# Kernel tuning notes

Hardware: AMD Instinct MI355X
Metric: run time of the kernel (lower is better)

Reference implementation:

```python
import jax, jax.numpy as jnp
from jax import lax
import numpy as np

B, T, U, P, K = 8192, 256, 64, 64, 2048

def setup_inputs() -> dict:
    key = jax.random.key(0)
    ku, ky, kw1, kw2 = jax.random.split(key, 4)
    u = jax.random.normal(ku, (B, T, U), dtype=jnp.float32)
    y0 = jax.random.normal(ky, (B, P), dtype=jnp.float32)
    W1 = jax.random.normal(kw1, (U + P, K), dtype=jnp.float32) * (1.0 / np.sqrt(U + P))
    b1 = jnp.zeros((K,), dtype=jnp.float32)
    W2 = jax.random.normal(kw2, (K, 1), dtype=jnp.float32) * (1.0 / np.sqrt(K))
    b2 = jnp.zeros((1,), dtype=jnp.float32)
    return {"u": u, "y0": y0, "W1": W1, "b1": b1, "W2": W2, "b2": b2}

def reference(u, y0, W1, b1, W2, b2):
    def step(y, u_t):
        # x: [B, U+P]
        x = jnp.concatenate([u_t, y], axis=1)
        h = jnp.tanh(x @ W1 + b1)          # [B, K]
        pred = h @ W2 + b2                 # [B, 1]
        # roll(shift=1)[:,1:] == y[:, :-1]; newest prediction goes to front
        y_new = jnp.concatenate([pred, y[:, :-1]], axis=1)  # [B, P]
        return y_new, pred

    u_t_first = jnp.swapaxes(u, 0, 1)      # [T, B, U]
    _, preds = lax.scan(step, y0, u_t_first)  # preds: [T, B, 1]
    return jnp.transpose(preds, (1, 0, 2))    # [B, T, 1]
```

## Files before the change

### kernel.cpp

```cpp
#include <hip/hip_runtime.h>
#include <hip/hip_fp16.h>
#include <cstdint>
#include <cstddef>

#define T_STEPS 256
#define K_DIM 2048
#define NCW 8
#define NT_W 8
#define REG_NT 4
#define LDS_NT 4

typedef _Float16 f16;
typedef _Float16 f16x8 __attribute__((ext_vector_type(8)));
typedef _Float16 f16x4 __attribute__((ext_vector_type(4)));
typedef _Float16 f16x2 __attribute__((ext_vector_type(2)));
typedef float f32x4 __attribute__((ext_vector_type(4)));

#define W1S_OFF 0
#define U_OFF   131072
#define Y_OFF   139264
#define PB_OFF  155648
#define SMEM_BYTES 157696

#define W1P_BYTES (128 * 4 * 64 * 16)
#define MBOX_OFF  W1P_BYTES
#define MBOX_BYTES (256 * 2 * 2 * 32 * 8)

__global__ void __launch_bounds__(64) prepack_w1(const float* __restrict__ W1,
                                                 f16* __restrict__ w1p) {
  int blk = blockIdx.x;
  int ntile = blk >> 2, ks = blk & 3;
  int lane = threadIdx.x;
  int col = ntile * 16 + (lane & 15);
  int kb = ks * 32 + ((lane >> 4) << 3);
  f16x8 pk;
#pragma unroll
  for (int i = 0; i < 8; ++i) pk[i] = (f16)W1[(size_t)(kb + i) * K_DIM + col];
  ((f16x8*)w1p)[(ntile * 4 + ks) * 64 + lane] = pk;
}

__global__ void __launch_bounds__(512, 2)
__attribute__((amdgpu_waves_per_eu(2, 2)))
rnn_fused(const float* __restrict__ u, const float* __restrict__ y0,
          const f16* __restrict__ w1p, const float* __restrict__ b1,
          const float* __restrict__ w2, const float* __restrict__ b2,
          float* __restrict__ out, unsigned long long* mbox)
{
  __shared__ __align__(16) char smem[SMEM_BYTES];
  f16x8* w1s     = (f16x8*)(smem + W1S_OFF);
  float* predbuf = (float*)(smem + PB_OFF);

  const int tid = threadIdx.x, lane = tid & 63, wave = tid >> 6;
  const int b = blockIdx.x;
  const int jj_ = b >> 3;
  const int half = jj_ & 1;
  const int pair = ((b & 7) << 4) | (jj_ >> 1);
  const int partner = b ^ 8;
  const int row0 = pair * 64;
  const int colbase = half * 1024;
  const float b2v = b2[0];
  const f16x8* w1pv = (const f16x8*)w1p;
  const float TWO_L = 2.885390081777927f;

  float b1x[NT_W], w2v[NT_W];
#pragma unroll
  for (int nt = 0; nt < NT_W; ++nt) {
    int col = colbase + wave * 128 + nt * 16 + (lane & 15);
    b1x[nt] = TWO_L * b1[col];
    w2v[nt] = w2[col];
  }

  float Chalf = 0.f;
  if (wave == 0) {
    float s = 0.f;
#pragma unroll
    for (int i = 0; i < 16; ++i) s += w2[colbase + lane * 16 + i];
    s += __shfl_xor(s, 1);  s += __shfl_xor(s, 2);  s += __shfl_xor(s, 4);
    s += __shfl_xor(s, 8);  s += __shfl_xor(s, 16); s += __shfl_xor(s, 32);
    Chalf = s;
  }

  f16x8 w1r[REG_NT * 4];
#pragma unroll
  for (int nt = 0; nt < REG_NT; ++nt)
#pragma unroll
    for (int ks = 0; ks < 4; ++ks)
      w1r[nt * 4 + ks] = w1pv[((half * 64 + wave * 8 + nt) * 4 + ks) * 64 + lane];
#pragma unroll
  for (int i = 0; i < REG_NT * 4; ++i) asm volatile("" : "+v"(w1r[i]));
#pragma unroll
  for (int nt = 0; nt < LDS_NT; ++nt)
#pragma unroll
    for (int ks = 0; ks < 4; ++ks)
      w1s[((wave * LDS_NT + nt) * 4 + ks) * 64 + lane] =
          w1pv[((half * 64 + wave * 8 + REG_NT + nt) * 4 + ks) * 64 + lane];

  const int r_i = tid >> 4;
  const int j0c = (tid & 15) * 4;
  const int sw_i = (r_i & 7) << 4;
  float4 upA, upB;
#pragma unroll
  for (int g = 0; g < 2; ++g) {
    int row = row0 + g * 32 + r_i;
    {
      float4 a = *(const float4*)(y0 + (size_t)row * 64 + j0c);
      f16x4 pk; pk[0] = (f16)a.x; pk[1] = (f16)a.y; pk[2] = (f16)a.z; pk[3] = (f16)a.w;
      *(f16x4*)(smem + Y_OFF + (g * 2 + 0) * 4096 + ((r_i * 128 + j0c * 2) ^ sw_i)) = pk;
    }
    {
      float4 a = *(const float4*)(u + ((size_t)row * T_STEPS + 0) * 64 + j0c);
      f16x4 pk; pk[0] = (f16)a.x; pk[1] = (f16)a.y; pk[2] = (f16)a.z; pk[3] = (f16)a.w;
      *(f16x4*)(smem + U_OFF + g * 4096 + ((r_i * 128 + j0c * 2) ^ sw_i)) = pk;
    }
    float4 p1 = *(const float4*)(u + ((size_t)row * T_STEPS + 1) * 64 + j0c);
    if (g == 0) upA = p1; else upB = p1;
  }
  __syncthreads();

  float contrib0 = 0.f, contrib1 = 0.f;

  auto region = [&](int g, int t) {
    const int gp = g ^ 1;
    const int t_p = (g == 1) ? t : t - 1;
    const int par = t & 1;
    const int par_p = t_p & 1;

    unsigned long long pv0 = 0;
    const unsigned long long* mb = nullptr;

    if (t_p >= 0) {
      if (wave == 0 && lane < 32) {
        float own = 0.f;
#pragma unroll
        for (int w = 0; w < NCW; ++w) own += predbuf[gp * 256 + w * 32 + lane];
        float c = fmaf(-2.0f, own, Chalf);
        if (gp == 0) contrib0 = c; else contrib1 = c;
        unsigned long long val =
            ((unsigned long long)(unsigned)(t_p + 1) << 32) |
            (unsigned long long)__builtin_bit_cast(unsigned, c);
        __hip_atomic_store(&mbox[((size_t)((b * 2 + gp) * 2 + par_p)) * 32 + lane], val,
                           __ATOMIC_RELAXED, __HIP_MEMORY_SCOPE_AGENT);
        mb = &mbox[((size_t)((partner * 2 + gp) * 2 + par_p)) * 32 + lane];
        pv0 = __hip_atomic_load(mb, __ATOMIC_RELAXED, __HIP_MEMORY_SCOPE_AGENT);
        asm volatile("" : "+v"(pv0));
      }
      {
        const char* yp = smem + Y_OFF + (gp * 2 + par_p) * 4096;
        char*       yn = smem + Y_OFF + (gp * 2 + (par_p ^ 1)) * 4096;
        f16x4 chB = *(const f16x4*)(yp + ((r_i * 128 + j0c * 2) ^ sw_i));
        char* dst = yn + ((r_i * 128 + j0c * 2) ^ sw_i);
        if (j0c) {
          f16x4 nw;
          nw[0] = *(const f16*)(yp + ((r_i * 128 + j0c * 2 - 2) ^ sw_i));
          nw[1] = chB[0]; nw[2] = chB[1]; nw[3] = chB[2];
          *(f16x4*)dst = nw;
        } else {
          *(f16*)(dst + 2) = chB[0];
          f16x2 hi; hi[0] = chB[1]; hi[1] = chB[2];
          *(f16x2*)(dst + 4) = hi;
        }
        if (t_p + 1 < T_STEPS) {
          float4 up = (gp == 0) ? upA : upB;
          f16x4 pk; pk[0] = (f16)up.x; pk[1] = (f16)up.y; pk[2] = (f16)up.z; pk[3] = (f16)up.w;
          *(f16x4*)(smem + U_OFF + gp * 4096 + ((r_i * 128 + j0c * 2) ^ sw_i)) = pk;
        }
        if (t_p + 2 < T_STEPS) {
          float4 p = *(const float4*)(
              u + ((size_t)(row0 + gp * 32 + r_i) * T_STEPS + (t_p + 2)) * 64 + j0c);
          if (gp == 0) upA = p; else upB = p;
        }
      }
    }

    const char* ubase = smem + U_OFF + g * 4096;
    const char* ybase = smem + Y_OFF + (g * 2 + par) * 4096;
    f16x8 af[2][4];
    {
      int koff = (lane >> 4) << 4;
#pragma unroll
      for (int mt = 0; mt < 2; ++mt) {
        int r = mt * 16 + (lane & 15);
        int base = r * 128 + koff, sw = (r & 7) << 4;
        af[mt][0] = *(const f16x8*)(ubase + (base ^ sw));
        af[mt][1] = *(const f16x8*)(ubase + ((base + 64) ^ sw));
        af[mt][2] = *(const f16x8*)(ybase + (base ^ sw));
        af[mt][3] = *(const f16x8*)(ybase + ((base + 64) ^ sw));
      }
    }

    auto mfma_nt = [&](int nt, f32x4* acc) {
      acc[0] = (f32x4){0.f, 0.f, 0.f, 0.f};
      acc[1] = (f32x4){0.f, 0.f, 0.f, 0.f};
      __builtin_amdgcn_s_setprio(1);
#pragma unroll
      for (int ks = 0; ks < 4; ++ks) {
        f16x8 bf = (nt < REG_NT)
                       ? w1r[nt * 4 + ks]
                       : w1s[((wave * LDS_NT + (nt - REG_NT)) * 4 + ks) * 64 + lane];
        acc[0] = __builtin_amdgcn_mfma_f32_16x16x32_f16(af[0][ks], bf, acc[0], 0, 0, 0);
        acc[1] = __builtin_amdgcn_mfma_f32_16x16x32_f16(af[1][ks], bf, acc[1], 0, 0, 0);
      }
      __builtin_amdgcn_s_setprio(0);
    };

    float predp[2][4];
#pragma unroll
    for (int mt = 0; mt < 2; ++mt)
#pragma unroll
      for (int jj = 0; jj < 4; ++jj) predp[mt][jj] = 0.f;

    auto epi = [&](int nt, f32x4* acc) {
#pragma unroll
      for (int mt = 0; mt < 2; ++mt)
#pragma unroll
        for (int jj = 0; jj < 4; ++jj) {
          float e  = __builtin_amdgcn_exp2f(fmaf(TWO_L, acc[mt][jj], b1x[nt]));
          float rr = __builtin_amdgcn_rcpf(1.0f + e);
          predp[mt][jj] = fmaf(w2v[nt], rr, predp[mt][jj]);
        }
    };

    f32x4 accA[2], accB[2];
    mfma_nt(0, accA);
    mfma_nt(1, accB);
    epi(0, accA); mfma_nt(2, accA);
    epi(1, accB); mfma_nt(3, accB);
    epi(2, accA); mfma_nt(4, accA);
    epi(3, accB); mfma_nt(5, accB);
    epi(4, accA); mfma_nt(6, accA);
    epi(5, accB); mfma_nt(7, accB);
    epi(6, accA);
    epi(7, accB);

#pragma unroll
    for (int mt = 0; mt < 2; ++mt)
#pragma unroll
      for (int jj = 0; jj < 4; ++jj) {
        float v = predp[mt][jj];
        v += __shfl_xor(v, 1); v += __shfl_xor(v, 2);
        v += __shfl_xor(v, 4); v += __shfl_xor(v, 8);
        if ((lane & 15) == 0)
          predbuf[g * 256 + wave * 32 + mt * 16 + ((lane >> 4) << 2) + jj] = v;
      }

    if (t_p >= 0 && wave == 0 && lane < 32) {
      const unsigned want = (unsigned)(t_p + 1);
      unsigned long long pv = pv0;
      while ((unsigned)(pv >> 32) != want)
        pv = __hip_atomic_load(mb, __ATOMIC_RELAXED, __HIP_MEMORY_SCOPE_AGENT);
      float pc = __builtin_bit_cast(float, (unsigned)(pv & 0xffffffffu));
      float ps = ((gp == 0) ? contrib0 : contrib1) + pc + b2v;
      if (t_p + 1 < T_STEPS)
        *(f16*)(smem + Y_OFF + (gp * 2 + ((t_p + 1) & 1)) * 4096 +
                ((lane * 128) ^ ((lane & 7) << 4))) = (f16)ps;
      if (half == 0)
        out[(size_t)(row0 + gp * 32 + lane) * T_STEPS + t_p] = ps;
    }
    __syncthreads();
  };

  for (int t = 0; t < T_STEPS; ++t) {
    region(0, t);
    region(1, t);
  }

  if (wave == 0 && lane < 32) {
    float own = 0.f;
#pragma unroll
    for (int w = 0; w < NCW; ++w) own += predbuf[1 * 256 + w * 32 + lane];
    float c1 = fmaf(-2.0f, own, Chalf);
    unsigned long long val =
        ((unsigned long long)(unsigned)T_STEPS << 32) |
        (unsigned long long)__builtin_bit_cast(unsigned, c1);
    __hip_atomic_store(&mbox[((size_t)((b * 2 + 1) * 2 + 1)) * 32 + lane], val,
                       __ATOMIC_RELAXED, __HIP_MEMORY_SCOPE_AGENT);
    const unsigned want = (unsigned)T_STEPS;
    unsigned long long pv;
    const unsigned long long* mb =
        &mbox[((size_t)((partner * 2 + 1) * 2 + 1)) * 32 + lane];
    do {
      pv = __hip_atomic_load(mb, __ATOMIC_RELAXED, __HIP_MEMORY_SCOPE_AGENT);
    } while ((unsigned)(pv >> 32) != want);
    float pc = __builtin_bit_cast(float, (unsigned)(pv & 0xffffffffu));
    float ps = c1 + pc + b2v;
    if (half == 0)
      out[(size_t)(row0 + 32 + lane) * T_STEPS + (T_STEPS - 1)] = ps;
  }
}

extern "C" void kernel_launch(void* const* d_in, const int* in_sizes, int n_in,
                              void* d_out, int out_size, void* d_ws, size_t ws_size,
                              hipStream_t stream) {
  const float* u  = (const float*)d_in[0];
  const float* y0 = (const float*)d_in[1];
  const float* W1 = (const float*)d_in[2];
  const float* b1 = (const float*)d_in[3];
  const float* W2 = (const float*)d_in[4];
  const float* b2 = (const float*)d_in[5];

  f16* w1p = (f16*)d_ws;
  unsigned long long* mbox = (unsigned long long*)((char*)d_ws + MBOX_OFF);

  hipMemsetAsync((char*)d_ws + MBOX_OFF, 0, MBOX_BYTES, stream);

  prepack_w1<<<512, 64, 0, stream>>>(W1, w1p);

  rnn_fused<<<256, 512, 0, stream>>>(u, y0, w1p, b1, W2, b2, (float*)d_out, mbox);
}
```

Measured before the change: 1.834 ms.

## Double workgroup to 1024 threads, halving per-wave column tiles

Each workgroup now runs 16 waves instead of 8. Each wave handles 4 column tiles of 16 instead of 8, with half of W1 kept in registers and half in LDS. The per-step y-shift and u-staging work is spread over twice as many threads using 2-element vectors. Each of the two interleaved row groups gets its own coordinator wave for the partner-mailbox exchange. The aim is more latency hiding per CU on the serial timestep chain, at the cost of a larger cross-wave reduction (16 partial sums) and barriers that now span 16 waves.

Measured after the change: 2.309 ms. +25.9%, slower.

```diff
diff --git a/kernel.cpp b/kernel.cpp
--- a/kernel.cpp
+++ b/kernel.cpp
@@ -5,10 +5,10 @@
 
 #define T_STEPS 256
 #define K_DIM 2048
-#define NCW 8
-#define NT_W 8
-#define REG_NT 4
-#define LDS_NT 4
+#define NW 16
+#define NT_W 4
+#define REG_NT 2
+#define LDS_NT 2
 
 typedef _Float16 f16;
 typedef _Float16 f16x8 __attribute__((ext_vector_type(8)));
@@ -20,7 +20,7 @@
 #define U_OFF   131072
 #define Y_OFF   139264
 #define PB_OFF  155648
-#define SMEM_BYTES 157696
+#define SMEM_BYTES 159744
 
 #define W1P_BYTES (128 * 4 * 64 * 16)
 #define MBOX_OFF  W1P_BYTES
@@ -39,8 +39,8 @@
   ((f16x8*)w1p)[(ntile * 4 + ks) * 64 + lane] = pk;
 }
 
-__global__ void __launch_bounds__(512, 2)
-__attribute__((amdgpu_waves_per_eu(2, 2)))
+__global__ void __launch_bounds__(1024, 4)
+__attribute__((amdgpu_waves_per_eu(4, 4)))
 rnn_fused(const float* __restrict__ u, const float* __restrict__ y0,
           const f16* __restrict__ w1p, const float* __restrict__ b1,
           const float* __restrict__ w2, const float* __restrict__ b2,
@@ -65,13 +65,13 @@
   float b1x[NT_W], w2v[NT_W];
 #pragma unroll
   for (int nt = 0; nt < NT_W; ++nt) {
-    int col = colbase + wave * 128 + nt * 16 + (lane & 15);
+    int col = colbase + wave * 64 + nt * 16 + (lane & 15);
     b1x[nt] = TWO_L * b1[col];
     w2v[nt] = w2[col];
   }
 
   float Chalf = 0.f;
-  if (wave == 0) {
+  if (wave < 2) {
     float s = 0.f;
 #pragma unroll
     for (int i = 0; i < 16; ++i) s += w2[colbase + lane * 16 + i];
@@ -85,7 +85,7 @@
   for (int nt = 0; nt < REG_NT; ++nt)
 #pragma unroll
     for (int ks = 0; ks < 4; ++ks)
-      w1r[nt * 4 + ks] = w1pv[((half * 64 + wave * 8 + nt) * 4 + ks) * 64 + lane];
+      w1r[nt * 4 + ks] = w1pv[((half * 64 + wave * 4 + nt) * 4 + ks) * 64 + lane];
 #pragma unroll
   for (int i = 0; i < REG_NT * 4; ++i) asm volatile("" : "+v"(w1r[i]));
 #pragma unroll
@@ -93,26 +93,26 @@
 #pragma unroll
     for (int ks = 0; ks < 4; ++ks)
       w1s[((wave * LDS_NT + nt) * 4 + ks) * 64 + lane] =
-          w1pv[((half * 64 + wave * 8 + REG_NT + nt) * 4 + ks) * 64 + lane];
-
-  const int r_i = tid >> 4;
-  const int j0c = (tid & 15) * 4;
+          w1pv[((half * 64 + wave * 4 + REG_NT + nt) * 4 + ks) * 64 + lane];
+
+  const int r_i = tid >> 5;
+  const int j0 = (tid & 31) * 2;
   const int sw_i = (r_i & 7) << 4;
-  float4 upA, upB;
+  float2 upA, upB;
 #pragma unroll
   for (int g = 0; g < 2; ++g) {
     int row = row0 + g * 32 + r_i;
     {
-      float4 a = *(const float4*)(y0 + (size_t)row * 64 + j0c);
-      f16x4 pk; pk[0] = (f16)a.x; pk[1] = (f16)a.y; pk[2] = (f16)a.z; pk[3] = (f16)a.w;
-      *(f16x4*)(smem + Y_OFF + (g * 2 + 0) * 4096 + ((r_i * 128 + j0c * 2) ^ sw_i)) = pk;
+      float2 a = *(const float2*)(y0 + (size_t)row * 64 + j0);
+      f16x2 pk; pk[0] = (f16)a.x; pk[1] = (f16)a.y;
+      *(f16x2*)(smem + Y_OFF + (g * 2 + 0) * 4096 + ((r_i * 128 + j0 * 2) ^ sw_i)) = pk;
     }
     {
-      float4 a = *(const float4*)(u + ((size_t)row * T_STEPS + 0) * 64 + j0c);
-      f16x4 pk; pk[0] = (f16)a.x; pk[1] = (f16)a.y; pk[2] = (f16)a.z; pk[3] = (f16)a.w;
-      *(f16x4*)(smem + U_OFF + g * 4096 + ((r_i * 128 + j0c * 2) ^ sw_i)) = pk;
-    }
-    float4 p1 = *(const float4*)(u + ((size_t)row * T_STEPS + 1) * 64 + j0c);
+      float2 a = *(const float2*)(u + ((size_t)row * T_STEPS + 0) * 64 + j0);
+      f16x2 pk; pk[0] = (f16)a.x; pk[1] = (f16)a.y;
+      *(f16x2*)(smem + U_OFF + g * 4096 + ((r_i * 128 + j0 * 2) ^ sw_i)) = pk;
+    }
+    float2 p1 = *(const float2*)(u + ((size_t)row * T_STEPS + 1) * 64 + j0);
     if (g == 0) upA = p1; else upB = p1;
   }
   __syncthreads();
@@ -124,15 +124,16 @@
     const int t_p = (g == 1) ? t : t - 1;
     const int par = t & 1;
     const int par_p = t_p & 1;
+    const int cw = gp;
 
     unsigned long long pv0 = 0;
     const unsigned long long* mb = nullptr;
 
     if (t_p >= 0) {
-      if (wave == 0 && lane < 32) {
+      if (wave == cw && lane < 32) {
         float own = 0.f;
 #pragma unroll
-        for (int w = 0; w < NCW; ++w) own += predbuf[gp * 256 + w * 32 + lane];
+        for (int w = 0; w < NW; ++w) own += predbuf[gp * 512 + w * 32 + lane];
         float c = fmaf(-2.0f, own, Chalf);
         if (gp == 0) contrib0 = c; else contrib1 = c;
         unsigned long long val =
@@ -147,26 +148,22 @@
       {
         const char* yp = smem + Y_OFF + (gp * 2 + par_p) * 4096;
         char*       yn = smem + Y_OFF + (gp * 2 + (par_p ^ 1)) * 4096;
-        f16x4 chB = *(const f16x4*)(yp + ((r_i * 128 + j0c * 2) ^ sw_i));
-        char* dst = yn + ((r_i * 128 + j0c * 2) ^ sw_i);
-        if (j0c) {
-          f16x4 nw;
-          nw[0] = *(const f16*)(yp + ((r_i * 128 + j0c * 2 - 2) ^ sw_i));
-          nw[1] = chB[0]; nw[2] = chB[1]; nw[3] = chB[2];
-          *(f16x4*)dst = nw;
+        f16 a1 = *(const f16*)(yp + ((r_i * 128 + j0 * 2) ^ sw_i));
+        if (j0) {
+          f16 a0 = *(const f16*)(yp + ((r_i * 128 + j0 * 2 - 2) ^ sw_i));
+          f16x2 nw; nw[0] = a0; nw[1] = a1;
+          *(f16x2*)(yn + ((r_i * 128 + j0 * 2) ^ sw_i)) = nw;
         } else {
-          *(f16*)(dst + 2) = chB[0];
-          f16x2 hi; hi[0] = chB[1]; hi[1] = chB[2];
-          *(f16x2*)(dst + 4) = hi;
+          *(f16*)(yn + ((r_i * 128 + 2) ^ sw_i)) = a1;
         }
         if (t_p + 1 < T_STEPS) {
-          float4 up = (gp == 0) ? upA : upB;
-          f16x4 pk; pk[0] = (f16)up.x; pk[1] = (f16)up.y; pk[2] = (f16)up.z; pk[3] = (f16)up.w;
-          *(f16x4*)(smem + U_OFF + gp * 4096 + ((r_i * 128 + j0c * 2) ^ sw_i)) = pk;
+          float2 up = (gp == 0) ? upA : upB;
+          f16x2 pk; pk[0] = (f16)up.x; pk[1] = (f16)up.y;
+          *(f16x2*)(smem + U_OFF + gp * 4096 + ((r_i * 128 + j0 * 2) ^ sw_i)) = pk;
         }
         if (t_p + 2 < T_STEPS) {
-          float4 p = *(const float4*)(
-              u + ((size_t)(row0 + gp * 32 + r_i) * T_STEPS + (t_p + 2)) * 64 + j0c);
+          float2 p = *(const float2*)(
+              u + ((size_t)(row0 + gp * 32 + r_i) * T_STEPS + (t_p + 2)) * 64 + j0);
           if (gp == 0) upA = p; else upB = p;
         }
       }
@@ -225,12 +222,8 @@
     mfma_nt(1, accB);
     epi(0, accA); mfma_nt(2, accA);
     epi(1, accB); mfma_nt(3, accB);
-    epi(2, accA); mfma_nt(4, accA);
-    epi(3, accB); mfma_nt(5, accB);
-    epi(4, accA); mfma_nt(6, accA);
-    epi(5, accB); mfma_nt(7, accB);
-    epi(6, accA);
-    epi(7, accB);
+    epi(2, accA);
+    epi(3, accB);
 
 #pragma unroll
     for (int mt = 0; mt < 2; ++mt)
@@ -240,10 +233,10 @@
         v += __shfl_xor(v, 1); v += __shfl_xor(v, 2);
         v += __shfl_xor(v, 4); v += __shfl_xor(v, 8);
         if ((lane & 15) == 0)
-          predbuf[g * 256 + wave * 32 + mt * 16 + ((lane >> 4) << 2) + jj] = v;
-      }
-
-    if (t_p >= 0 && wave == 0 && lane < 32) {
+          predbuf[g * 512 + wave * 32 + mt * 16 + ((lane >> 4) << 2) + jj] = v;
+      }
+
+    if (t_p >= 0 && wave == cw && lane < 32) {
       const unsigned want = (unsigned)(t_p + 1);
       unsigned long long pv = pv0;
       while ((unsigned)(pv >> 32) != want)
@@ -264,10 +257,10 @@
     region(1, t);
   }
 
-  if (wave == 0 && lane < 32) {
+  if (wave == 1 && lane < 32) {
     float own = 0.f;
 #pragma unroll
-    for (int w = 0; w < NCW; ++w) own += predbuf[1 * 256 + w * 32 + lane];
+    for (int w = 0; w < NW; ++w) own += predbuf[1 * 512 + w * 32 + lane];
     float c1 = fmaf(-2.0f, own, Chalf);
     unsigned long long val =
         ((unsigned long long)(unsigned)T_STEPS << 32) |
@@ -305,5 +298,5 @@
 
   prepack_w1<<<512, 64, 0, stream>>>(W1, w1p);
 
-  rnn_fused<<<256, 512, 0, stream>>>(u, y0, w1p, b1, W2, b2, (float*)d_out, mbox);
+  rnn_fused<<<256, 1024, 0, stream>>>(u, y0, w1p, b1, W2, b2, (float*)d_out, mbox);
 }
```

## Spread cross-block prediction combine and mailbox exchange across all waves

Applied to the files above, without the earlier changes.

The per-row reduction of wave partial predictions and the mailbox store, load and spin with the partner block move off wave 0 alone. Each of the 8 waves now handles 4 rows, with 8 lanes per row summing partials through shuffles. This shortens the serial tail on the critical path of each step, since one wave no longer does 8 LDS reads plus all 32 atomic exchanges. The cost is that every wave now performs cross-block atomics and spin-waits, which may add memory traffic and contention on the mailbox lines.

After: 2.197 ms. 19.8% more time.

```diff
diff --git a/kernel.cpp b/kernel.cpp
--- a/kernel.cpp
+++ b/kernel.cpp
@@ -62,6 +62,10 @@
   const f16x8* w1pv = (const f16x8*)w1p;
   const float TWO_L = 2.885390081777927f;
 
+  const int cpart = lane & 7;
+  const int crow  = wave * 4 + (lane >> 3);
+  const bool cpost = (lane < 32) && (cpart == 0);
+
   float b1x[NT_W], w2v[NT_W];
 #pragma unroll
   for (int nt = 0; nt < NT_W; ++nt) {
@@ -70,8 +74,8 @@
     w2v[nt] = w2[col];
   }
 
-  float Chalf = 0.f;
-  if (wave == 0) {
+  float Chalf;
+  {
     float s = 0.f;
 #pragma unroll
     for (int i = 0; i < 16; ++i) s += w2[colbase + lane * 16 + i];
@@ -117,8 +121,6 @@
   }
   __syncthreads();
 
-  float contrib0 = 0.f, contrib1 = 0.f;
-
   auto region = [&](int g, int t) {
     const int gp = g ^ 1;
     const int t_p = (g == 1) ? t : t - 1;
@@ -127,22 +129,24 @@
 
     unsigned long long pv0 = 0;
     const unsigned long long* mb = nullptr;
+    float creg = 0.f;
 
     if (t_p >= 0) {
-      if (wave == 0 && lane < 32) {
+      {
         float own = 0.f;
-#pragma unroll
-        for (int w = 0; w < NCW; ++w) own += predbuf[gp * 256 + w * 32 + lane];
-        float c = fmaf(-2.0f, own, Chalf);
-        if (gp == 0) contrib0 = c; else contrib1 = c;
-        unsigned long long val =
-            ((unsigned long long)(unsigned)(t_p + 1) << 32) |
-            (unsigned long long)__builtin_bit_cast(unsigned, c);
-        __hip_atomic_store(&mbox[((size_t)((b * 2 + gp) * 2 + par_p)) * 32 + lane], val,
-                           __ATOMIC_RELAXED, __HIP_MEMORY_SCOPE_AGENT);
-        mb = &mbox[((size_t)((partner * 2 + gp) * 2 + par_p)) * 32 + lane];
-        pv0 = __hip_atomic_load(mb, __ATOMIC_RELAXED, __HIP_MEMORY_SCOPE_AGENT);
-        asm volatile("" : "+v"(pv0));
+        if (lane < 32) own = predbuf[gp * 256 + cpart * 32 + crow];
+        own += __shfl_xor(own, 1); own += __shfl_xor(own, 2); own += __shfl_xor(own, 4);
+        if (cpost) {
+          creg = fmaf(-2.0f, own, Chalf);
+          unsigned long long val =
+              ((unsigned long long)(unsigned)(t_p + 1) << 32) |
+              (unsigned long long)__builtin_bit_cast(unsigned, creg);
+          __hip_atomic_store(&mbox[((size_t)((b * 2 + gp) * 2 + par_p)) * 32 + crow], val,
+                             __ATOMIC_RELAXED, __HIP_MEMORY_SCOPE_AGENT);
+          mb = &mbox[((size_t)((partner * 2 + gp) * 2 + par_p)) * 32 + crow];
+          pv0 = __hip_atomic_load(mb, __ATOMIC_RELAXED, __HIP_MEMORY_SCOPE_AGENT);
+          asm volatile("" : "+v"(pv0));
+        }
       }
       {
         const char* yp = smem + Y_OFF + (gp * 2 + par_p) * 4096;
@@ -243,18 +247,18 @@
           predbuf[g * 256 + wave * 32 + mt * 16 + ((lane >> 4) << 2) + jj] = v;
       }
 
-    if (t_p >= 0 && wave == 0 && lane < 32) {
+    if (t_p >= 0 && cpost) {
       const unsigned want = (unsigned)(t_p + 1);
       unsigned long long pv = pv0;
       while ((unsigned)(pv >> 32) != want)
         pv = __hip_atomic_load(mb, __ATOMIC_RELAXED, __HIP_MEMORY_SCOPE_AGENT);
       float pc = __builtin_bit_cast(float, (unsigned)(pv & 0xffffffffu));
-      float ps = ((gp == 0) ? contrib0 : contrib1) + pc + b2v;
+      float ps = creg + pc + b2v;
       if (t_p + 1 < T_STEPS)
         *(f16*)(smem + Y_OFF + (gp * 2 + ((t_p + 1) & 1)) * 4096 +
-                ((lane * 128) ^ ((lane & 7) << 4))) = (f16)ps;
+                ((crow * 128) ^ ((crow & 7) << 4))) = (f16)ps;
       if (half == 0)
-        out[(size_t)(row0 + gp * 32 + lane) * T_STEPS + t_p] = ps;
+        out[(size_t)(row0 + gp * 32 + crow) * T_STEPS + t_p] = ps;
     }
     __syncthreads();
   };
@@ -264,27 +268,29 @@
     region(1, t);
   }
 
-  if (wave == 0 && lane < 32) {
+  {
     float own = 0.f;
-#pragma unroll
-    for (int w = 0; w < NCW; ++w) own += predbuf[1 * 256 + w * 32 + lane];
-    float c1 = fmaf(-2.0f, own, Chalf);
-    unsigned long long val =
-        ((unsigned long long)(unsigned)T_STEPS << 32) |
-        (unsigned long long)__builtin_bit_cast(unsigned, c1);
-    __hip_atomic_store(&mbox[((size_t)((b * 2 + 1) * 2 + 1)) * 32 + lane], val,
-                       __ATOMIC_RELAXED, __HIP_MEMORY_SCOPE_AGENT);
-    const unsigned want = (unsigned)T_STEPS;
-    unsigned long long pv;
-    const unsigned long long* mb =
-        &mbox[((size_t)((partner * 2 + 1) * 2 + 1)) * 32 + lane];
-    do {
-      pv = __hip_atomic_load(mb, __ATOMIC_RELAXED, __HIP_MEMORY_SCOPE_AGENT);
-    } while ((unsigned)(pv >> 32) != want);
-    float pc = __builtin_bit_cast(float, (unsigned)(pv & 0xffffffffu));
-    float ps = c1 + pc + b2v;
-    if (half == 0)
-      out[(size_t)(row0 + 32 + lane) * T_STEPS + (T_STEPS - 1)] = ps;
+    if (lane < 32) own = predbuf[1 * 256 + cpart * 32 + crow];
+    own += __shfl_xor(own, 1); own += __shfl_xor(own, 2); own += __shfl_xor(own, 4);
+    if (cpost) {
+      float c1 = fmaf(-2.0f, own, Chalf);
+      unsigned long long val =
+          ((unsigned long long)(unsigned)T_STEPS << 32) |
+          (unsigned long long)__builtin_bit_cast(unsigned, c1);
+      __hip_atomic_store(&mbox[((size_t)((b * 2 + 1) * 2 + 1)) * 32 + crow], val,
+                         __ATOMIC_RELAXED, __HIP_MEMORY_SCOPE_AGENT);
+      const unsigned want = (unsigned)T_STEPS;
+      unsigned long long pv;
+      const unsigned long long* mbf =
+          &mbox[((size_t)((partner * 2 + 1) * 2 + 1)) * 32 + crow];
+      do {
+        pv = __hip_atomic_load(mbf, __ATOMIC_RELAXED, __HIP_MEMORY_SCOPE_AGENT);
+      } while ((unsigned)(pv >> 32) != want);
+      float pc = __builtin_bit_cast(float, (unsigned)(pv & 0xffffffffu));
+      float ps = c1 + pc + b2v;
+      if (half == 0)
+        out[(size_t)(row0 + 32 + crow) * T_STEPS + (T_STEPS - 1)] = ps;
+    }
   }
 }
 
```
